# Optimization experiments

Measured on AMD Instinct MI355X. Metric: run time of the kernel, lower is better.

## Reference

```python
import jax, jax.numpy as jnp
import numpy as np

B, T, DIM = 2, 2048, 2048
N_HEADS, N_KV_HEADS = 32, 8
HEAD_DIM = DIM // N_HEADS          # 64
N_REP = N_HEADS // N_KV_HEADS      # 4
ROPE_THETA = 10000.0


def setup_inputs() -> dict:
    key = jax.random.key(0)
    ks = jax.random.split(key, 5)
    x = jax.random.normal(ks[0], (B, T, DIM), dtype=jnp.float32)
    # RoPE frequencies: freqs_cis[t, j] = exp(i * t * theta^{-2j/head_dim})
    inv_freq = 1.0 / (ROPE_THETA ** (jnp.arange(0, HEAD_DIM, 2, dtype=jnp.float32) / HEAD_DIM))
    angles = jnp.arange(T, dtype=jnp.float32)[:, None] * inv_freq[None, :]  # [T, HEAD_DIM//2]
    cos, sin = jnp.cos(angles), jnp.sin(angles)
    s = 0.02
    wq = jax.random.normal(ks[1], (N_HEADS * HEAD_DIM, DIM), dtype=jnp.float32) * s
    wk = jax.random.normal(ks[2], (N_KV_HEADS * HEAD_DIM, DIM), dtype=jnp.float32) * s
    wv = jax.random.normal(ks[3], (N_KV_HEADS * HEAD_DIM, DIM), dtype=jnp.float32) * s
    wo = jax.random.normal(ks[4], (DIM, DIM), dtype=jnp.float32) * s
    return {"x": x, "cos": cos, "sin": sin, "wq": wq, "wk": wk, "wv": wv, "wo": wo}


def _apply_rope(t, cos, sin):
    # t: [B, T, H, D]; cos/sin: [T, D//2]. Complex multiply on interleaved pairs.
    b, tt, h, d = t.shape
    tr = t.reshape(b, tt, h, d // 2, 2)
    t0, t1 = tr[..., 0], tr[..., 1]
    c = cos[None, :, None, :]
    s = sin[None, :, None, :]
    o0 = t0 * c - t1 * s
    o1 = t0 * s + t1 * c
    return jnp.stack([o0, o1], axis=-1).reshape(b, tt, h, d)


def reference(x, cos, sin, wq, wk, wv, wo):
    Bs, Ts, C = x.shape
    # Projections (nn.Linear, no bias): y = x @ W^T
    q = jnp.einsum('btc,oc->bto', x, wq).reshape(Bs, Ts, N_HEADS, HEAD_DIM)
    k = jnp.einsum('btc,oc->bto', x, wk).reshape(Bs, Ts, N_KV_HEADS, HEAD_DIM)
    v = jnp.einsum('btc,oc->bto', x, wv).reshape(Bs, Ts, N_KV_HEADS, HEAD_DIM)
    q = _apply_rope(q, cos[:Ts], sin[:Ts])
    k = _apply_rope(k, cos[:Ts], sin[:Ts])
    # [B, H, T, D]; GQA: broadcast kv heads via grouped einsum instead of repeat.
    q = q.transpose(0, 2, 1, 3).reshape(Bs, N_KV_HEADS, N_REP, Ts, HEAD_DIM)
    k = k.transpose(0, 2, 1, 3)  # [B, Hkv, T, D]
    v = v.transpose(0, 2, 1, 3)
    scale = 1.0 / jnp.sqrt(jnp.asarray(HEAD_DIM, dtype=x.dtype))
    scores = jnp.einsum('bgrqd,bgkd->bgrqk', q, k) * scale  # [B, Hkv, rep, T, T]
    causal = jnp.tril(jnp.ones((Ts, Ts), dtype=bool))
    scores = jnp.where(causal, scores, jnp.finfo(scores.dtype).min)
    attn = jax.nn.softmax(scores, axis=-1)
    y = jnp.einsum('bgrqk,bgkd->bgrqd', attn, v)           # [B, Hkv, rep, T, D]
    y = y.reshape(Bs, N_HEADS, Ts, HEAD_DIM).transpose(0, 2, 1, 3).reshape(Bs, Ts, C)
    return jnp.einsum('btc,oc->bto', y, wo)
```

## Files before the change

kernel.cpp:

```cpp
#include <hip/hip_runtime.h>

typedef __bf16 bf16;
typedef __attribute__((ext_vector_type(8))) __bf16 bf16x8;
typedef __attribute__((ext_vector_type(4))) __bf16 bf16x4;
typedef __attribute__((ext_vector_type(4))) float f32x4;

constexpr int T_SEQ = 2048;
constexpr int DIM   = 2048;
constexpr int NH    = 32;
constexpr int NKV   = 8;
constexpr int HD    = 64;
constexpr int QKV_N = DIM + 2 * NKV * HD;
constexpr int MROWS = 2 * T_SEQ;

__global__ void cast_all_kernel(const float* __restrict__ x,
                                const float* __restrict__ wq, const float* __restrict__ wk,
                                const float* __restrict__ wv, const float* __restrict__ wo,
                                bf16* __restrict__ xb, bf16* __restrict__ wqkv,
                                bf16* __restrict__ wob) {
  int stride = gridDim.x * blockDim.x;
  for (int g = blockIdx.x * blockDim.x + threadIdx.x; g < 4718592; g += stride) {
    const float* src; bf16* dst; int off;
    if (g < 2097152)      { src = x;  dst = xb;             off = g; }
    else if (g < 3145728) { src = wq; dst = wqkv;           off = g - 2097152; }
    else if (g < 3407872) { src = wk; dst = wqkv + 4194304; off = g - 3145728; }
    else if (g < 3670016) { src = wv; dst = wqkv + 5242880; off = g - 3407872; }
    else                  { src = wo; dst = wob;            off = g - 3670016; }
    float4 v = *(const float4*)(src + (size_t)off * 4);
    bf16x4 o = { (bf16)v.x, (bf16)v.y, (bf16)v.z, (bf16)v.w };
    *(bf16x4*)(dst + (size_t)off * 4) = o;
  }
}

__device__ inline void rect_decode(int orig, int& bmi, int& bni) {
  int c = orig & 7, i = orig >> 3;
  bmi = (c & 1) * 8 + (i & 7);
  bni = (c >> 1) * 4 + (i >> 3);
}

__global__ __launch_bounds__(512) void gemm256(const bf16* __restrict__ A,
                                               const bf16* __restrict__ W,
                                               float* __restrict__ C,
                                               int N, int K) {
  constexpr int BM = 256, BN = 128, BK = 64;
  __shared__ __attribute__((aligned(16))) bf16 Ab[3][BM * BK];
  __shared__ __attribute__((aligned(16))) bf16 Bb[3][BN * BK];
  const int tid = threadIdx.x, lane = tid & 63, wave = tid >> 6;
  const int l15 = lane & 15, l4 = lane >> 4;
  int bmi, bni;
  rect_decode(blockIdx.x, bmi, bni);
  const int bm = bmi * BM, bn = bni * BN;
  const int wm = (wave >> 1) * 64, wn = (wave & 1) * 64;

  f32x4 acc[4][4] = {};

  const int NT = K / BK;
  auto stage = [&](int s, int k0) {
    #pragma unroll
    for (int i = 0; i < 4; ++i) {
      int c = i * 512 + tid;
      int row = c >> 3;
      int gc = ((c & 7) ^ (row & 7)) << 3;
      __builtin_amdgcn_global_load_lds(
          (const __attribute__((address_space(1))) unsigned int*)(A + (size_t)(bm + row) * K + k0 + gc),
          (__attribute__((address_space(3))) unsigned int*)(&Ab[s][0] + c * 8), 16, 0, 0);
    }
    #pragma unroll
    for (int i = 0; i < 2; ++i) {
      int c = i * 512 + tid;
      int row = c >> 3;
      int gc = ((c & 7) ^ (row & 7)) << 3;
      __builtin_amdgcn_global_load_lds(
          (const __attribute__((address_space(1))) unsigned int*)(W + (size_t)(bn + row) * K + k0 + gc),
          (__attribute__((address_space(3))) unsigned int*)(&Bb[s][0] + c * 8), 16, 0, 0);
    }
  };

  stage(0, 0);
  stage(1, BK);

  int d = 0;
  for (int t = 0; t < NT; ++t) {
    if (t + 1 < NT) { asm volatile("s_waitcnt vmcnt(6)" ::: "memory"); }
    else            { asm volatile("s_waitcnt vmcnt(0)" ::: "memory"); }
    __builtin_amdgcn_s_barrier();

    bf16x8 af[2][4], bfr[2][4];
    #pragma unroll
    for (int kk = 0; kk < 2; ++kk) {
      #pragma unroll
      for (int mi = 0; mi < 4; ++mi) {
        int row = wm + mi * 16 + l15;
        af[kk][mi] = *(const bf16x8*)((const char*)&Ab[d][0] + row * 128 +
                                      (((kk * 4 + l4) ^ (row & 7)) << 4));
      }
      #pragma unroll
      for (int ni = 0; ni < 4; ++ni) {
        int row = wn + ni * 16 + l15;
        bfr[kk][ni] = *(const bf16x8*)((const char*)&Bb[d][0] + row * 128 +
                                       (((kk * 4 + l4) ^ (row & 7)) << 4));
      }
    }

    if (t + 2 < NT) {
      int s = d + 2; if (s >= 3) s -= 3;
      stage(s, (t + 2) * BK);
    }

    __builtin_amdgcn_s_setprio(1);
    #pragma unroll
    for (int kk = 0; kk < 2; ++kk)
      #pragma unroll
      for (int mi = 0; mi < 4; ++mi)
        #pragma unroll
        for (int ni = 0; ni < 4; ++ni)
          acc[mi][ni] = __builtin_amdgcn_mfma_f32_16x16x32_bf16(af[kk][mi], bfr[kk][ni],
                                                                acc[mi][ni], 0, 0, 0);
    __builtin_amdgcn_s_setprio(0);

    ++d; if (d == 3) d = 0;
  }

  #pragma unroll
  for (int mi = 0; mi < 4; ++mi)
    #pragma unroll
    for (int ni = 0; ni < 4; ++ni) {
      size_t row = (size_t)bm + wm + mi * 16 + l4 * 4;
      int col = bn + wn + ni * 16 + l15;
      #pragma unroll
      for (int r = 0; r < 4; ++r)
        C[(row + r) * N + col] = acc[mi][ni][r];
    }
}

__global__ __launch_bounds__(512, 1) void gemm192(const bf16* __restrict__ A,
                                                  const bf16* __restrict__ W,
                                                  bf16* __restrict__ C,
                                                  const float* __restrict__ cs,
                                                  const float* __restrict__ sn) {
  constexpr int BM = 256, BN = 192, BK = 64, N = QKV_N, K = DIM;
  __shared__ __attribute__((aligned(16))) bf16 Ab[3][BM * BK];
  __shared__ __attribute__((aligned(16))) bf16 Bb[2][BN * BK];
  const int tid = threadIdx.x, lane = tid & 63, wave = tid >> 6;
  const int l15 = lane & 15, l4 = lane >> 4;
  int bmi, bni;
  rect_decode(blockIdx.x, bmi, bni);
  const int bm = bmi * BM, bn = bni * BN;
  const int wm = (wave >> 1) * 64, wn = (wave & 1) * 96;

  f32x4 acc[4][6] = {};

  constexpr int NT = K / BK;
  auto stageA = [&](int s, int k0) {
    #pragma unroll
    for (int i = 0; i < 4; ++i) {
      int c = i * 512 + tid;
      int row = c >> 3;
      int gc = ((c & 7) ^ (row & 7)) << 3;
      __builtin_amdgcn_global_load_lds(
          (const __attribute__((address_space(1))) unsigned int*)(A + (size_t)(bm + row) * K + k0 + gc),
          (__attribute__((address_space(3))) unsigned int*)(&Ab[s][0] + c * 8), 16, 0, 0);
    }
  };
  auto stageB = [&](int s, int k0) {
    #pragma unroll
    for (int i = 0; i < 3; ++i) {
      int c = i * 512 + tid;
      int row = c >> 3;
      int gc = ((c & 7) ^ (row & 7)) << 3;
      __builtin_amdgcn_global_load_lds(
          (const __attribute__((address_space(1))) unsigned int*)(W + (size_t)(bn + row) * K + k0 + gc),
          (__attribute__((address_space(3))) unsigned int*)(&Bb[s][0] + c * 8), 16, 0, 0);
    }
  };

  stageA(0, 0);
  stageB(0, 0);
  stageA(1, BK);

  for (int t = 0; t < NT; ++t) {
    const int d3 = t % 3, db = t & 1;
    if (t + 1 < NT) { asm volatile("s_waitcnt vmcnt(4)" ::: "memory"); }
    else            { asm volatile("s_waitcnt vmcnt(0)" ::: "memory"); }
    __builtin_amdgcn_s_barrier();

    bf16x8 af[2][4], bfr[2][6];
    #pragma unroll
    for (int kk = 0; kk < 2; ++kk) {
      #pragma unroll
      for (int mi = 0; mi < 4; ++mi) {
        int row = wm + mi * 16 + l15;
        af[kk][mi] = *(const bf16x8*)((const char*)&Ab[d3][0] + row * 128 +
                                      (((kk * 4 + l4) ^ (row & 7)) << 4));
      }
      #pragma unroll
      for (int ni = 0; ni < 6; ++ni) {
        int row = wn + ni * 16 + l15;
        bfr[kk][ni] = *(const bf16x8*)((const char*)&Bb[db][0] + row * 128 +
                                       (((kk * 4 + l4) ^ (row & 7)) << 4));
      }
    }

    if (t + 1 < NT) stageB(db ^ 1, (t + 1) * BK);
    if (t + 2 < NT) { int s = d3 + 2; if (s >= 3) s -= 3; stageA(s, (t + 2) * BK); }

    __builtin_amdgcn_s_setprio(1);
    #pragma unroll
    for (int kk = 0; kk < 2; ++kk)
      #pragma unroll
      for (int mi = 0; mi < 4; ++mi)
        #pragma unroll
        for (int ni = 0; ni < 6; ++ni)
          acc[mi][ni] = __builtin_amdgcn_mfma_f32_16x16x32_bf16(af[kk][mi], bfr[kk][ni],
                                                                acc[mi][ni], 0, 0, 0);
    __builtin_amdgcn_s_setprio(0);
  }

  const bool odd = (l15 & 1);
  #pragma unroll
  for (int ni = 0; ni < 6; ++ni) {
    if (bn + wn + ni * 16 < 2560) {
      int col = bn + wn + ni * 16 + l15;
      int ip = (col & 63) >> 1;
      #pragma unroll
      for (int mi = 0; mi < 4; ++mi) {
        int row0 = wm + mi * 16 + l4 * 4;
        #pragma unroll
        for (int r = 0; r < 4; ++r) {
          int tpos = (bm + row0 + r) & (T_SEQ - 1);
          float c = cs[tpos * 32 + ip];
          float s = sn[tpos * 32 + ip];
          float a = acc[mi][ni][r];
          float p = __shfl_xor(a, 1);
          acc[mi][ni][r] = odd ? (p * s + a * c) : (a * c - p * s);
        }
      }
    }
  }

  #pragma unroll
  for (int mi = 0; mi < 4; ++mi)
    #pragma unroll
    for (int ni = 0; ni < 6; ++ni) {
      size_t row = (size_t)bm + wm + mi * 16 + l4 * 4;
      int col = bn + wn + ni * 16 + l15;
      #pragma unroll
      for (int r = 0; r < 4; ++r)
        C[(row + r) * N + col] = (bf16)acc[mi][ni][r];
    }
}

__global__ __launch_bounds__(512, 2) void attn_kernel(const bf16* __restrict__ qkv,
                                                      bf16* __restrict__ y) {
  const int h = blockIdx.x, b = blockIdx.z;
  const int strip = 15 - blockIdx.y;
  const int g = h >> 2;
  const int tid = threadIdx.x, lane = tid & 63, wave = tid >> 6;
  const int l15 = lane & 15, l4 = lane >> 4;
  const int qbase = strip * 128 + wave * 16;

  __shared__ __attribute__((aligned(16))) bf16 Kb[2][128 * 64];
  __shared__ __attribute__((aligned(16))) bf16 VTs[2][2][64 * 64];
  __shared__ __attribute__((aligned(16))) bf16 Pb[8][16 * 64];

  constexpr float SCALE2 = 0.125f * 1.44269504088896f;
  constexpr float THR_RAW = 8.0f / SCALE2;
  constexpr int VOFF = DIM + NKV * HD;

  const bf16 one1 = (bf16)1.0f;
  const bf16x8 ones = { one1, one1, one1, one1, one1, one1, one1, one1 };

  bf16x8 qf[2];
  {
    const bf16* qp = qkv + ((size_t)b * T_SEQ + qbase + l15) * QKV_N + h * HD + l4 * 8;
    qf[0] = *(const bf16x8*)(qp);
    qf[1] = *(const bf16x8*)(qp + 32);
  }

  f32x4 oacc[4] = {};
  f32x4 lacc = {};
  float m_run = -INFINITY;
  const int qg = qbase + l15;

  const int nt = strip + 1;
  const size_t kvbase = (size_t)b * T_SEQ;
  const int vwoff = ((lane * 128 + wave * 16) ^ ((lane & 7) << 4));

  {
    #pragma unroll
    for (int i = 0; i < 2; ++i) {
      int chunk = i * 512 + tid;
      int row = chunk >> 3;
      int csrc = ((chunk & 7) << 3) ^ ((row & 7) << 3);
      __builtin_amdgcn_global_load_lds(
          (const __attribute__((address_space(1))) unsigned int*)
              (qkv + (kvbase + row) * QKV_N + DIM + g * HD + csrc),
          (__attribute__((address_space(3))) unsigned int*)(&Kb[0][0] + chunk * 8), 16, 0, 0);
    }
    #pragma unroll
    for (int hf = 0; hf < 2; ++hf) {
      const bf16* vp = qkv + (kvbase + hf * 64 + wave * 8) * QKV_N + VOFF + g * HD + lane;
      bf16x8 vr;
      #pragma unroll
      for (int j = 0; j < 8; ++j) vr[j] = vp[(size_t)j * QKV_N];
      *(bf16x8*)((char*)&VTs[0][hf][0] + vwoff) = vr;
    }
    asm volatile("s_waitcnt vmcnt(0)" ::: "memory");
    __syncthreads();
  }

  int cur = 0;
  for (int kt = 0; kt < nt; ++kt) {
    const bool has_next = (kt + 1) < nt;
    bf16x8 vr0, vr1;
    if (has_next) {
      #pragma unroll
      for (int i = 0; i < 2; ++i) {
        int chunk = i * 512 + tid;
        int row = chunk >> 3;
        int csrc = ((chunk & 7) << 3) ^ ((row & 7) << 3);
        __builtin_amdgcn_global_load_lds(
            (const __attribute__((address_space(1))) unsigned int*)
                (qkv + (kvbase + (kt + 1) * 128 + row) * QKV_N + DIM + g * HD + csrc),
            (__attribute__((address_space(3))) unsigned int*)(&Kb[cur ^ 1][0] + chunk * 8), 16, 0, 0);
      }
      const bf16* vp0 = qkv + (kvbase + (kt + 1) * 128 + wave * 8) * QKV_N + VOFF + g * HD + lane;
      const bf16* vp1 = vp0 + (size_t)64 * QKV_N;
      #pragma unroll
      for (int j = 0; j < 8; ++j) vr0[j] = vp0[(size_t)j * QKV_N];
      #pragma unroll
      for (int j = 0; j < 8; ++j) vr1[j] = vp1[(size_t)j * QKV_N];
    }

    const bf16* kb = &Kb[cur][0];
    const bool diag = (kt == strip);

    #pragma unroll
    for (int hf = 0; hf < 2; ++hf) {
      if (diag && hf == 1 && wave < 4) continue;

      f32x4 z[4];
      #pragma unroll
      for (int nt4 = 0; nt4 < 4; ++nt4) z[nt4] = (f32x4){0.f, 0.f, 0.f, 0.f};
      __builtin_amdgcn_s_setprio(1);
      #pragma unroll
      for (int nt4 = 0; nt4 < 4; ++nt4)
        #pragma unroll
        for (int kk = 0; kk < 2; ++kk) {
          bf16x8 kf = *(const bf16x8*)((const char*)kb +
              (((hf * 64 + nt4 * 16 + l15) * 128 + (kk * 32 + l4 * 8) * 2) ^ ((l15 & 7) << 4)));
          z[nt4] = __builtin_amdgcn_mfma_f32_16x16x32_bf16(kf, qf[kk], z[nt4], 0, 0, 0);
        }
      __builtin_amdgcn_s_setprio(0);

      if (diag) {
        #pragma unroll
        for (int nt4 = 0; nt4 < 4; ++nt4)
          #pragma unroll
          for (int r = 0; r < 4; ++r)
            if (kt * 128 + hf * 64 + nt4 * 16 + l4 * 4 + r > qg) z[nt4][r] = -INFINITY;
      }

      float a0 = fmaxf(fmaxf(z[0][0], z[0][1]), z[0][2]);
      float a1 = fmaxf(fmaxf(z[0][3], z[1][0]), z[1][1]);
      float a2 = fmaxf(fmaxf(z[1][2], z[1][3]), z[2][0]);
      float a3 = fmaxf(fmaxf(z[2][1], z[2][2]), z[2][3]);
      float a4 = fmaxf(fmaxf(z[3][0], z[3][1]), z[3][2]);
      float b0 = fmaxf(fmaxf(a0, a1), a2);
      float b1 = fmaxf(fmaxf(a3, a4), z[3][3]);
      float vm = fmaxf(b0, b1);
      vm = fmaxf(vm, __shfl_xor(vm, 16));
      vm = fmaxf(vm, __shfl_xor(vm, 32));

      if (!__all(vm - m_run <= THR_RAW)) {
        float mnew = fmaxf(m_run, vm);
        float alpha = __builtin_amdgcn_exp2f((m_run - mnew) * SCALE2);
        #pragma unroll
        for (int r = 0; r < 4; ++r) lacc[r] *= alpha;
        #pragma unroll
        for (int dt = 0; dt < 4; ++dt)
          #pragma unroll
          for (int r = 0; r < 4; ++r) oacc[dt][r] *= alpha;
        m_run = mnew;
      }
      const float ms = m_run * SCALE2;

      #pragma unroll
      for (int nt4 = 0; nt4 < 4; ++nt4)
        #pragma unroll
        for (int r = 0; r < 4; ++r)
          z[nt4][r] = __builtin_amdgcn_exp2f(__builtin_fmaf(z[nt4][r], SCALE2, -ms));

      bf16* pbw = &Pb[wave][0];
      #pragma unroll
      for (int nt4 = 0; nt4 < 4; ++nt4) {
        bf16x4 pk = { (bf16)z[nt4][0], (bf16)z[nt4][1], (bf16)z[nt4][2], (bf16)z[nt4][3] };
        *(bf16x4*)((char*)pbw + ((l15 * 128 + nt4 * 32 + l4 * 8) ^ ((l15 & 7) << 4))) = pk;
      }

      const bf16* vt = &VTs[cur][hf][0];
      __builtin_amdgcn_s_setprio(1);
      #pragma unroll
      for (int kk = 0; kk < 2; ++kk) {
        bf16x8 pf = *(const bf16x8*)((const char*)pbw +
            ((l15 * 128 + kk * 64 + l4 * 16) ^ ((l15 & 7) << 4)));
        lacc = __builtin_amdgcn_mfma_f32_16x16x32_bf16(ones, pf, lacc, 0, 0, 0);
        #pragma unroll
        for (int dt = 0; dt < 4; ++dt) {
          bf16x8 vf = *(const bf16x8*)((const char*)vt +
              (((dt * 16 + l15) * 128 + (kk * 32 + l4 * 8) * 2) ^ ((l15 & 7) << 4)));
          oacc[dt] = __builtin_amdgcn_mfma_f32_16x16x32_bf16(vf, pf, oacc[dt], 0, 0, 0);
        }
      }
      __builtin_amdgcn_s_setprio(0);
    }

    if (has_next) {
      *(bf16x8*)((char*)&VTs[cur ^ 1][0][0] + vwoff) = vr0;
      *(bf16x8*)((char*)&VTs[cur ^ 1][1][0] + vwoff) = vr1;
      __syncthreads();
      cur ^= 1;
    }
  }

  {
    float linv = __builtin_amdgcn_rcpf(lacc[0]);
    bf16* yp = y + ((size_t)b * T_SEQ + qbase + l15) * DIM + h * HD + l4 * 4;
    #pragma unroll
    for (int dt = 0; dt < 4; ++dt) {
      bf16x4 ov = { (bf16)(oacc[dt][0] * linv), (bf16)(oacc[dt][1] * linv),
                    (bf16)(oacc[dt][2] * linv), (bf16)(oacc[dt][3] * linv) };
      *(bf16x4*)(yp + dt * 16) = ov;
    }
  }
}

extern "C" void kernel_launch(void* const* d_in, const int* in_sizes, int n_in,
                              void* d_out, int out_size, void* d_ws, size_t ws_size,
                              hipStream_t stream) {
  const float* x    = (const float*)d_in[0];
  const float* cosb = (const float*)d_in[1];
  const float* sinb = (const float*)d_in[2];
  const float* wq   = (const float*)d_in[3];
  const float* wk   = (const float*)d_in[4];
  const float* wv   = (const float*)d_in[5];
  const float* wo   = (const float*)d_in[6];
  float* out = (float*)d_out;

  bf16* xb   = (bf16*)d_ws;
  bf16* wqkv = xb + (size_t)MROWS * DIM;
  bf16* wob  = wqkv + (size_t)QKV_N * DIM;
  bf16* qkv  = wob + (size_t)DIM * DIM;
  bf16* y    = qkv + (size_t)MROWS * QKV_N;

  cast_all_kernel<<<2048, 256, 0, stream>>>(x, wq, wk, wv, wo, xb, wqkv, wob);

  gemm192<<<256, 512, 0, stream>>>(xb, wqkv, qkv, cosb, sinb);

  attn_kernel<<<dim3(NH, 16, 2), 512, 0, stream>>>(qkv, y);

  gemm256<<<256, 512, 0, stream>>>(y, wob, out, DIM, DIM);
}
```

Baseline: 160.8 us.

## Process two query heads per attention block to share K/V tile loads

Each attention workgroup now handles two query heads of the same KV group. Every K/V tile staged in shared memory feeds twice as many MFMAs, which halves the K/V global loads and LDS fills per head. The grid shrinks to half as many blocks (512 instead of 1024). In exchange each wave holds twice the accumulators and Q fragments, raising register pressure and possibly lowering occupancy under the existing launch bounds.

```diff
diff --git a/kernel.cpp b/kernel.cpp
--- a/kernel.cpp
+++ b/kernel.cpp
@@ -252,9 +252,9 @@
 
 __global__ __launch_bounds__(512, 2) void attn_kernel(const bf16* __restrict__ qkv,
                                                       bf16* __restrict__ y) {
-  const int h = blockIdx.x, b = blockIdx.z;
+  const int hp = blockIdx.x, b = blockIdx.z;
   const int strip = 15 - blockIdx.y;
-  const int g = h >> 2;
+  const int h0 = 2 * hp, g = hp >> 1;
   const int tid = threadIdx.x, lane = tid & 63, wave = tid >> 6;
   const int l15 = lane & 15, l4 = lane >> 4;
   const int qbase = strip * 128 + wave * 16;
@@ -270,16 +270,18 @@
   const bf16 one1 = (bf16)1.0f;
   const bf16x8 ones = { one1, one1, one1, one1, one1, one1, one1, one1 };
 
-  bf16x8 qf[2];
+  bf16x8 qfA[2], qfB[2];
   {
-    const bf16* qp = qkv + ((size_t)b * T_SEQ + qbase + l15) * QKV_N + h * HD + l4 * 8;
-    qf[0] = *(const bf16x8*)(qp);
-    qf[1] = *(const bf16x8*)(qp + 32);
-  }
-
-  f32x4 oacc[4] = {};
-  f32x4 lacc = {};
-  float m_run = -INFINITY;
+    const bf16* qp = qkv + ((size_t)b * T_SEQ + qbase + l15) * QKV_N + h0 * HD + l4 * 8;
+    qfA[0] = *(const bf16x8*)(qp);
+    qfA[1] = *(const bf16x8*)(qp + 32);
+    qfB[0] = *(const bf16x8*)(qp + HD);
+    qfB[1] = *(const bf16x8*)(qp + HD + 32);
+  }
+
+  f32x4 oaccA[4] = {}, oaccB[4] = {};
+  f32x4 laccA = {}, laccB = {};
+  float mA = -INFINITY, mB = -INFINITY;
   const int qg = qbase + l15;
 
   const int nt = strip + 1;
@@ -339,9 +341,12 @@
     for (int hf = 0; hf < 2; ++hf) {
       if (diag && hf == 1 && wave < 4) continue;
 
-      f32x4 z[4];
-      #pragma unroll
-      for (int nt4 = 0; nt4 < 4; ++nt4) z[nt4] = (f32x4){0.f, 0.f, 0.f, 0.f};
+      f32x4 zA[4], zB[4];
+      #pragma unroll
+      for (int nt4 = 0; nt4 < 4; ++nt4) {
+        zA[nt4] = (f32x4){0.f, 0.f, 0.f, 0.f};
+        zB[nt4] = (f32x4){0.f, 0.f, 0.f, 0.f};
+      }
       __builtin_amdgcn_s_setprio(1);
       #pragma unroll
       for (int nt4 = 0; nt4 < 4; ++nt4)
@@ -349,7 +354,8 @@
         for (int kk = 0; kk < 2; ++kk) {
           bf16x8 kf = *(const bf16x8*)((const char*)kb +
               (((hf * 64 + nt4 * 16 + l15) * 128 + (kk * 32 + l4 * 8) * 2) ^ ((l15 & 7) << 4)));
-          z[nt4] = __builtin_amdgcn_mfma_f32_16x16x32_bf16(kf, qf[kk], z[nt4], 0, 0, 0);
+          zA[nt4] = __builtin_amdgcn_mfma_f32_16x16x32_bf16(kf, qfA[kk], zA[nt4], 0, 0, 0);
+          zB[nt4] = __builtin_amdgcn_mfma_f32_16x16x32_bf16(kf, qfB[kk], zB[nt4], 0, 0, 0);
         }
       __builtin_amdgcn_s_setprio(0);
 
@@ -358,58 +364,101 @@
         for (int nt4 = 0; nt4 < 4; ++nt4)
           #pragma unroll
           for (int r = 0; r < 4; ++r)
-            if (kt * 128 + hf * 64 + nt4 * 16 + l4 * 4 + r > qg) z[nt4][r] = -INFINITY;
-      }
-
-      float a0 = fmaxf(fmaxf(z[0][0], z[0][1]), z[0][2]);
-      float a1 = fmaxf(fmaxf(z[0][3], z[1][0]), z[1][1]);
-      float a2 = fmaxf(fmaxf(z[1][2], z[1][3]), z[2][0]);
-      float a3 = fmaxf(fmaxf(z[2][1], z[2][2]), z[2][3]);
-      float a4 = fmaxf(fmaxf(z[3][0], z[3][1]), z[3][2]);
-      float b0 = fmaxf(fmaxf(a0, a1), a2);
-      float b1 = fmaxf(fmaxf(a3, a4), z[3][3]);
-      float vm = fmaxf(b0, b1);
-      vm = fmaxf(vm, __shfl_xor(vm, 16));
-      vm = fmaxf(vm, __shfl_xor(vm, 32));
-
-      if (!__all(vm - m_run <= THR_RAW)) {
-        float mnew = fmaxf(m_run, vm);
-        float alpha = __builtin_amdgcn_exp2f((m_run - mnew) * SCALE2);
-        #pragma unroll
-        for (int r = 0; r < 4; ++r) lacc[r] *= alpha;
-        #pragma unroll
-        for (int dt = 0; dt < 4; ++dt)
-          #pragma unroll
-          for (int r = 0; r < 4; ++r) oacc[dt][r] *= alpha;
-        m_run = mnew;
-      }
-      const float ms = m_run * SCALE2;
-
-      #pragma unroll
-      for (int nt4 = 0; nt4 < 4; ++nt4)
-        #pragma unroll
-        for (int r = 0; r < 4; ++r)
-          z[nt4][r] = __builtin_amdgcn_exp2f(__builtin_fmaf(z[nt4][r], SCALE2, -ms));
+            if (kt * 128 + hf * 64 + nt4 * 16 + l4 * 4 + r > qg) {
+              zA[nt4][r] = -INFINITY;
+              zB[nt4][r] = -INFINITY;
+            }
+      }
 
       bf16* pbw = &Pb[wave][0];
-      #pragma unroll
-      for (int nt4 = 0; nt4 < 4; ++nt4) {
-        bf16x4 pk = { (bf16)z[nt4][0], (bf16)z[nt4][1], (bf16)z[nt4][2], (bf16)z[nt4][3] };
-        *(bf16x4*)((char*)pbw + ((l15 * 128 + nt4 * 32 + l4 * 8) ^ ((l15 & 7) << 4))) = pk;
+      bf16x8 pfA[2], pfB[2];
+
+      {
+        float a0 = fmaxf(fmaxf(zA[0][0], zA[0][1]), zA[0][2]);
+        float a1 = fmaxf(fmaxf(zA[0][3], zA[1][0]), zA[1][1]);
+        float a2 = fmaxf(fmaxf(zA[1][2], zA[1][3]), zA[2][0]);
+        float a3 = fmaxf(fmaxf(zA[2][1], zA[2][2]), zA[2][3]);
+        float a4 = fmaxf(fmaxf(zA[3][0], zA[3][1]), zA[3][2]);
+        float vm = fmaxf(fmaxf(fmaxf(a0, a1), a2), fmaxf(fmaxf(a3, a4), zA[3][3]));
+        vm = fmaxf(vm, __shfl_xor(vm, 16));
+        vm = fmaxf(vm, __shfl_xor(vm, 32));
+        if (!__all(vm - mA <= THR_RAW)) {
+          float mnew = fmaxf(mA, vm);
+          float alpha = __builtin_amdgcn_exp2f((mA - mnew) * SCALE2);
+          #pragma unroll
+          for (int r = 0; r < 4; ++r) laccA[r] *= alpha;
+          #pragma unroll
+          for (int dt = 0; dt < 4; ++dt)
+            #pragma unroll
+            for (int r = 0; r < 4; ++r) oaccA[dt][r] *= alpha;
+          mA = mnew;
+        }
+        const float ms = mA * SCALE2;
+        #pragma unroll
+        for (int nt4 = 0; nt4 < 4; ++nt4)
+          #pragma unroll
+          for (int r = 0; r < 4; ++r)
+            zA[nt4][r] = __builtin_amdgcn_exp2f(__builtin_fmaf(zA[nt4][r], SCALE2, -ms));
+        #pragma unroll
+        for (int nt4 = 0; nt4 < 4; ++nt4) {
+          bf16x4 pk = { (bf16)zA[nt4][0], (bf16)zA[nt4][1], (bf16)zA[nt4][2], (bf16)zA[nt4][3] };
+          *(bf16x4*)((char*)pbw + ((l15 * 128 + nt4 * 32 + l4 * 8) ^ ((l15 & 7) << 4))) = pk;
+        }
+        #pragma unroll
+        for (int kk = 0; kk < 2; ++kk)
+          pfA[kk] = *(const bf16x8*)((const char*)pbw +
+              ((l15 * 128 + kk * 64 + l4 * 16) ^ ((l15 & 7) << 4)));
+      }
+
+      {
+        float a0 = fmaxf(fmaxf(zB[0][0], zB[0][1]), zB[0][2]);
+        float a1 = fmaxf(fmaxf(zB[0][3], zB[1][0]), zB[1][1]);
+        float a2 = fmaxf(fmaxf(zB[1][2], zB[1][3]), zB[2][0]);
+        float a3 = fmaxf(fmaxf(zB[2][1], zB[2][2]), zB[2][3]);
+        float a4 = fmaxf(fmaxf(zB[3][0], zB[3][1]), zB[3][2]);
+        float vm = fmaxf(fmaxf(fmaxf(a0, a1), a2), fmaxf(fmaxf(a3, a4), zB[3][3]));
+        vm = fmaxf(vm, __shfl_xor(vm, 16));
+        vm = fmaxf(vm, __shfl_xor(vm, 32));
+        if (!__all(vm - mB <= THR_RAW)) {
+          float mnew = fmaxf(mB, vm);
+          float alpha = __builtin_amdgcn_exp2f((mB - mnew) * SCALE2);
+          #pragma unroll
+          for (int r = 0; r < 4; ++r) laccB[r] *= alpha;
+          #pragma unroll
+          for (int dt = 0; dt < 4; ++dt)
+            #pragma unroll
+            for (int r = 0; r < 4; ++r) oaccB[dt][r] *= alpha;
+          mB = mnew;
+        }
+        const float ms = mB * SCALE2;
+        #pragma unroll
+        for (int nt4 = 0; nt4 < 4; ++nt4)
+          #pragma unroll
+          for (int r = 0; r < 4; ++r)
+            zB[nt4][r] = __builtin_amdgcn_exp2f(__builtin_fmaf(zB[nt4][r], SCALE2, -ms));
+        #pragma unroll
+        for (int nt4 = 0; nt4 < 4; ++nt4) {
+          bf16x4 pk = { (bf16)zB[nt4][0], (bf16)zB[nt4][1], (bf16)zB[nt4][2], (bf16)zB[nt4][3] };
+          *(bf16x4*)((char*)pbw + ((l15 * 128 + nt4 * 32 + l4 * 8) ^ ((l15 & 7) << 4))) = pk;
+        }
+        #pragma unroll
+        for (int kk = 0; kk < 2; ++kk)
+          pfB[kk] = *(const bf16x8*)((const char*)pbw +
+              ((l15 * 128 + kk * 64 + l4 * 16) ^ ((l15 & 7) << 4)));
       }
 
       const bf16* vt = &VTs[cur][hf][0];
       __builtin_amdgcn_s_setprio(1);
       #pragma unroll
       for (int kk = 0; kk < 2; ++kk) {
-        bf16x8 pf = *(const bf16x8*)((const char*)pbw +
-            ((l15 * 128 + kk * 64 + l4 * 16) ^ ((l15 & 7) << 4)));
-        lacc = __builtin_amdgcn_mfma_f32_16x16x32_bf16(ones, pf, lacc, 0, 0, 0);
+        laccA = __builtin_amdgcn_mfma_f32_16x16x32_bf16(ones, pfA[kk], laccA, 0, 0, 0);
+        laccB = __builtin_amdgcn_mfma_f32_16x16x32_bf16(ones, pfB[kk], laccB, 0, 0, 0);
         #pragma unroll
         for (int dt = 0; dt < 4; ++dt) {
           bf16x8 vf = *(const bf16x8*)((const char*)vt +
               (((dt * 16 + l15) * 128 + (kk * 32 + l4 * 8) * 2) ^ ((l15 & 7) << 4)));
-          oacc[dt] = __builtin_amdgcn_mfma_f32_16x16x32_bf16(vf, pf, oacc[dt], 0, 0, 0);
+          oaccA[dt] = __builtin_amdgcn_mfma_f32_16x16x32_bf16(vf, pfA[kk], oaccA[dt], 0, 0, 0);
+          oaccB[dt] = __builtin_amdgcn_mfma_f32_16x16x32_bf16(vf, pfB[kk], oaccB[dt], 0, 0, 0);
         }
       }
       __builtin_amdgcn_s_setprio(0);
@@ -424,13 +473,17 @@
   }
 
   {
-    float linv = __builtin_amdgcn_rcpf(lacc[0]);
-    bf16* yp = y + ((size_t)b * T_SEQ + qbase + l15) * DIM + h * HD + l4 * 4;
+    float linvA = __builtin_amdgcn_rcpf(laccA[0]);
+    float linvB = __builtin_amdgcn_rcpf(laccB[0]);
+    bf16* yp = y + ((size_t)b * T_SEQ + qbase + l15) * DIM + h0 * HD + l4 * 4;
     #pragma unroll
     for (int dt = 0; dt < 4; ++dt) {
-      bf16x4 ov = { (bf16)(oacc[dt][0] * linv), (bf16)(oacc[dt][1] * linv),
-                    (bf16)(oacc[dt][2] * linv), (bf16)(oacc[dt][3] * linv) };
-      *(bf16x4*)(yp + dt * 16) = ov;
+      bf16x4 ovA = { (bf16)(oaccA[dt][0] * linvA), (bf16)(oaccA[dt][1] * linvA),
+                     (bf16)(oaccA[dt][2] * linvA), (bf16)(oaccA[dt][3] * linvA) };
+      bf16x4 ovB = { (bf16)(oaccB[dt][0] * linvB), (bf16)(oaccB[dt][1] * linvB),
+                     (bf16)(oaccB[dt][2] * linvB), (bf16)(oaccB[dt][3] * linvB) };
+      *(bf16x4*)(yp + dt * 16) = ovA;
+      *(bf16x4*)(yp + HD + dt * 16) = ovB;
     }
   }
 }
@@ -457,7 +510,7 @@
 
   gemm192<<<256, 512, 0, stream>>>(xb, wqkv, qkv, cosb, sinb);
 
-  attn_kernel<<<dim3(NH, 16, 2), 512, 0, stream>>>(qkv, y);
+  attn_kernel<<<dim3(NH / 2, 16, 2), 512, 0, stream>>>(qkv, y);
 
   gemm256<<<256, 512, 0, stream>>>(y, wob, out, DIM, DIM);
 }
```

Result: slower. 180.2 us (+12.1%).
